# Kernel optimization log

Measured on AMD Instinct MI355X. Metric: run time of the kernel, lower is better.

Reference implementation:

```python
import jax, jax.numpy as jnp
import numpy as np

D_MODEL = 1024


def setup_inputs() -> dict:
    key = jax.random.key(0)
    ks = jax.random.split(key, 7)
    x = jax.random.normal(ks[0], (4, 2048, D_MODEL), dtype=jnp.float32)
    scale = 1.0 / np.sqrt(D_MODEL)
    Wq = jax.random.normal(ks[1], (D_MODEL, D_MODEL), dtype=jnp.float32) * scale
    bq = jnp.zeros((D_MODEL,), dtype=jnp.float32)
    Wk = jax.random.normal(ks[2], (D_MODEL, D_MODEL), dtype=jnp.float32) * scale
    bk = jnp.zeros((D_MODEL,), dtype=jnp.float32)
    Wv = jax.random.normal(ks[3], (D_MODEL, D_MODEL), dtype=jnp.float32) * scale
    bv = jnp.zeros((D_MODEL,), dtype=jnp.float32)
    return {"x": x, "Wq": Wq, "bq": bq, "Wk": Wk, "bk": bk, "Wv": Wv, "bv": bv}


def reference(x, Wq, bq, Wk, bk, Wv, bv):
    # Linear layers: y = x @ W^T + b (torch nn.Linear convention)
    q = jnp.einsum("bsd,ed->bse", x, Wq) + bq
    k = jnp.einsum("bsd,ed->bse", x, Wk) + bk
    v = jnp.einsum("bsd,ed->bse", x, Wv) + bv
    d_k = q.shape[-1]
    inv_sqrt_dk = 1.0 / jnp.sqrt(jnp.float32(d_k))
    # [B, S, S] score matrix, softmax over keys, then AV
    score = jnp.einsum("bqd,bkd->bqk", q, k) * inv_sqrt_dk
    attn = jax.nn.softmax(score, axis=-1)
    out = jnp.einsum("bqk,bkd->bqd", attn, v)
    return out
```

## Files before the change

### kernel.cpp

```cpp
#include <hip/hip_runtime.h>
#include <hip/hip_bf16.h>


typedef __hip_bfloat16 bf16;
typedef __attribute__((ext_vector_type(8))) short bf16x8;
typedef __attribute__((ext_vector_type(4))) float f32x4;
typedef __attribute__((ext_vector_type(4))) short short4v;

__device__ __forceinline__ void gload16(const bf16* g, bf16* l) {
  __builtin_amdgcn_global_load_lds(
      (const __attribute__((address_space(1))) void*)g,
      (__attribute__((address_space(3))) void*)l, 16, 0, 0);
}

__global__ __launch_bounds__(256)
void cast_f32_to_bf16(const float* __restrict__ in, bf16* __restrict__ out) {
  long i = ((long)blockIdx.x * blockDim.x + threadIdx.x) * 4;
  float4 f = *(const float4*)(in + i);
  bf16 tmp[4];
  tmp[0] = __float2bfloat16(f.x);
  tmp[1] = __float2bfloat16(f.y);
  tmp[2] = __float2bfloat16(f.z);
  tmp[3] = __float2bfloat16(f.w);
  *(short4v*)(out + i) = *(short4v*)tmp;
}

__global__ __launch_bounds__(256)
void cast3_f32_to_bf16(const float* __restrict__ w0, const float* __restrict__ w1,
                       const float* __restrict__ w2, bf16* __restrict__ out) {
  const float* src = (blockIdx.y == 0) ? w0 : (blockIdx.y == 1) ? w1 : w2;
  long i = ((long)blockIdx.x * blockDim.x + threadIdx.x) * 4;
  float4 f = *(const float4*)(src + i);
  bf16 tmp[4];
  tmp[0] = __float2bfloat16(f.x);
  tmp[1] = __float2bfloat16(f.y);
  tmp[2] = __float2bfloat16(f.z);
  tmp[3] = __float2bfloat16(f.w);
  *(short4v*)(out + (long)blockIdx.y * 1024 * 1024 + i) = *(short4v*)tmp;
}

template<int OMODE>
__global__ __launch_bounds__(256, 3)
void gemm_bt(const bf16* __restrict__ A, const bf16* __restrict__ Bt,
             const float* __restrict__ b0, const float* __restrict__ b1,
             const float* __restrict__ b2, void* __restrict__ Cout,
             int K, int lda, int ldb, int ldc, float scale,
             long sA, long sB, long sC)
{
  __shared__ __align__(16) bf16 As[128 * 64];
  __shared__ __align__(16) bf16 Bs[128 * 64];
  const int tid = threadIdx.x;
  const int z = blockIdx.z;
  const bf16* Ab = A + (long)z * sA;
  const bf16* Bb = Bt + (long)z * sB;
  const long bm = (long)blockIdx.x * 128;
  const long bn = (long)blockIdx.y * 128;
  const int wid = tid >> 6;
  const int lane = tid & 63;
  const int wr = (wid >> 1) * 64;
  const int wc = (wid & 1) * 64;
  const int l15 = lane & 15;
  const int kg = lane >> 4;

  f32x4 acc[4][4];
#pragma unroll
  for (int m = 0; m < 4; ++m)
#pragma unroll
    for (int n = 0; n < 4; ++n)
      acc[m][n] = (f32x4){0.f, 0.f, 0.f, 0.f};

  for (int k0 = 0; k0 < K; k0 += 64) {
#pragma unroll
    for (int i = 0; i < 4; ++i) {
      const int c = (i << 8) + tid;
      const int r = c >> 3;
      const int j = (c & 7) ^ (r & 7);
      const int ldsch = (i << 8) + (wid << 6);
      gload16(Ab + (long)(bm + r) * lda + k0 + (j << 3), As + ldsch * 8);
      gload16(Bb + (long)(bn + r) * ldb + k0 + (j << 3), Bs + ldsch * 8);
    }
    __syncthreads();
#pragma unroll
    for (int kk = 0; kk < 2; ++kk) {
      bf16x8 af[4], bfv[4];
#pragma unroll
      for (int m = 0; m < 4; ++m) {
        const int row_l = wr + (m << 4) + l15;
        const int js = ((kk << 2) + kg) ^ (row_l & 7);
        af[m] = *(const bf16x8*)&As[(row_l << 6) + (js << 3)];
      }
#pragma unroll
      for (int n = 0; n < 4; ++n) {
        const int row_l = wc + (n << 4) + l15;
        const int js = ((kk << 2) + kg) ^ (row_l & 7);
        bfv[n] = *(const bf16x8*)&Bs[(row_l << 6) + (js << 3)];
      }
#pragma unroll
      for (int m = 0; m < 4; ++m)
#pragma unroll
        for (int n = 0; n < 4; ++n)
          acc[m][n] = __builtin_amdgcn_mfma_f32_16x16x32_bf16(
              af[m], bfv[n], acc[m][n], 0, 0, 0);
    }
    __syncthreads();
  }

#pragma unroll
  for (int m = 0; m < 4; ++m) {
    const long row0 = bm + wr + (m << 4) + (kg << 2);
#pragma unroll
    for (int n = 0; n < 4; ++n) {
      const long col = bn + wc + (n << 4) + l15;
      if constexpr (OMODE == 0) {
        float* C = (float*)Cout + (long)z * sC;
#pragma unroll
        for (int rr = 0; rr < 4; ++rr)
          C[(row0 + rr) * ldc + col] = acc[m][n][rr] * scale;
      } else if constexpr (OMODE == 1) {
        bf16* C = (bf16*)Cout + (long)z * sC;
#pragma unroll
        for (int rr = 0; rr < 4; ++rr)
          C[(row0 + rr) * ldc + col] = __float2bfloat16(acc[m][n][rr] * scale);
      } else {
        const float* bias = (z == 0) ? b0 : (z == 1) ? b1 : b2;
        const float bias_v = bias[col];
        if (z < 2) {
          bf16* C = (bf16*)Cout + (long)z * 8192 * 1024;
#pragma unroll
          for (int rr = 0; rr < 4; ++rr)
            C[(row0 + rr) * 1024 + col] =
                __float2bfloat16(acc[m][n][rr] + bias_v);
        } else {
          bf16* C = (bf16*)Cout + 2L * 8192 * 1024;
          const long bb = row0 >> 11;
          const long s0 = row0 & 2047;
          bf16 tmp[4];
#pragma unroll
          for (int rr = 0; rr < 4; ++rr)
            tmp[rr] = __float2bfloat16(acc[m][n][rr] + bias_v);
          *(short4v*)&C[(bb * 1024 + col) * 2048 + s0] = *(short4v*)tmp;
        }
      }
    }
  }
}

__global__ __launch_bounds__(256)
void softmax_bf16(bf16* __restrict__ S) {
  bf16* row = S + (size_t)blockIdx.x * 2048;
  const int tid = threadIdx.x;
  __shared__ float redA[4], redB[4];
  bf16x8 in = *(const bf16x8*)(row + (tid << 3));
  float v[8];
  float mx = -1e30f;
#pragma unroll
  for (int i = 0; i < 8; ++i) {
    v[i] = __bfloat162float(((const bf16*)&in)[i]);
    mx = fmaxf(mx, v[i]);
  }
#pragma unroll
  for (int o = 32; o; o >>= 1) mx = fmaxf(mx, __shfl_xor(mx, o));
  if ((tid & 63) == 0) redA[tid >> 6] = mx;
  __syncthreads();
  mx = fmaxf(fmaxf(redA[0], redA[1]), fmaxf(redA[2], redA[3]));
  float sum = 0.f;
#pragma unroll
  for (int i = 0; i < 8; ++i) {
    v[i] = __expf(v[i] - mx);
    sum += v[i];
  }
#pragma unroll
  for (int o = 32; o; o >>= 1) sum += __shfl_xor(sum, o);
  if ((tid & 63) == 0) redB[tid >> 6] = sum;
  __syncthreads();
  sum = redB[0] + redB[1] + redB[2] + redB[3];
  const float inv = 1.f / sum;
  bf16 tmp[8];
#pragma unroll
  for (int i = 0; i < 8; ++i) tmp[i] = __float2bfloat16(v[i] * inv);
  *(bf16x8*)(row + (tid << 3)) = *(bf16x8*)tmp;
}

extern "C" void kernel_launch(void* const* d_in, const int* in_sizes, int n_in,
                              void* d_out, int out_size, void* d_ws, size_t ws_size,
                              hipStream_t stream) {
  const float* x  = (const float*)d_in[0];
  const float* Wq = (const float*)d_in[1];
  const float* bq = (const float*)d_in[2];
  const float* Wk = (const float*)d_in[3];
  const float* bk = (const float*)d_in[4];
  const float* Wv = (const float*)d_in[5];
  const float* bv = (const float*)d_in[6];
  float* out = (float*)d_out;

  const int B = 4, S = 2048, D = 1024;
  const int M = B * S;

  bf16* xb  = (bf16*)d_ws;
  bf16* wqb = xb + (size_t)M * D;
  bf16* qb  = wqb + 3 * (size_t)D * D;
  bf16* kb  = qb + (size_t)M * D;
  bf16* vtb = kb + (size_t)M * D;
  bf16* sc  = vtb + (size_t)M * D;

  size_t avail = ws_size - ((size_t)((char*)sc - (char*)d_ws));
  int nb = (int)(avail / ((size_t)S * S * 2));
  if (nb > B) nb = B;
  if (nb < 1) nb = 1;

  cast_f32_to_bf16<<<dim3(M * D / 1024), 256, 0, stream>>>(x, xb);
  cast3_f32_to_bf16<<<dim3(D * D / 1024, 3), 256, 0, stream>>>(Wq, Wk, Wv, wqb);

  gemm_bt<3><<<dim3(M / 128, D / 128, 3), 256, 0, stream>>>(
      xb, wqb, bq, bk, bv, qb, D, D, D, D, 1.f, 0, (long)D * D, 0);

  const float iscale = 1.0f / 32.0f;
  for (int g = 0; g < B; g += nb) {
    const int gn = (g + nb <= B) ? nb : (B - g);
    gemm_bt<1><<<dim3(S / 128, S / 128, gn), 256, 0, stream>>>(
        qb + (size_t)g * S * D, kb + (size_t)g * S * D, nullptr, nullptr, nullptr,
        sc, D, D, D, S, iscale, (long)S * D, (long)S * D, (long)S * S);
    softmax_bf16<<<dim3(gn * S), 256, 0, stream>>>(sc);
    gemm_bt<0><<<dim3(S / 128, D / 128, gn), 256, 0, stream>>>(
        sc, vtb + (size_t)g * D * S, nullptr, nullptr, nullptr,
        out + (size_t)g * S * D, S, S, S, D, 1.f,
        (long)S * S, (long)D * S, (long)S * D);
  }
}
```

Measured before the change: 169.7 us.

## Triple-buffer GEMM with 256x128 tiles and 512-thread blocks

Replaces the single-buffered 128x128 GEMM with a 256x128-tile kernel that uses 8 waves and a three-stage LDS ring. Global-to-LDS loads for tile t+2 are issued before computing tile t, with explicit vmcnt waits and barriers, so memory latency overlaps MFMA work. The QKV projection now runs as one flat grid over the concatenated 3*D output columns rather than a z-batched launch. The cost is 144KB of LDS per block, which limits occupancy to one block per CU. Each wave also now handles an 8x2 MFMA fragment layout with less B reuse.

```diff
diff --git a/kernel.cpp b/kernel.cpp
--- a/kernel.cpp
+++ b/kernel.cpp
@@ -12,6 +12,10 @@
       (const __attribute__((address_space(1))) void*)g,
       (__attribute__((address_space(3))) void*)l, 16, 0, 0);
 }
+
+#define WAITV(N) asm volatile("s_waitcnt vmcnt(" #N ")" ::: "memory")
+#define SCHED0   __builtin_amdgcn_sched_barrier(0)
+#define BAR      __builtin_amdgcn_s_barrier()
 
 __global__ __launch_bounds__(256)
 void cast_f32_to_bf16(const float* __restrict__ in, bf16* __restrict__ out) {
@@ -40,97 +44,127 @@
 }
 
 template<int OMODE>
-__global__ __launch_bounds__(256, 3)
-void gemm_bt(const bf16* __restrict__ A, const bf16* __restrict__ Bt,
-             const float* __restrict__ b0, const float* __restrict__ b1,
-             const float* __restrict__ b2, void* __restrict__ Cout,
-             int K, int lda, int ldb, int ldc, float scale,
-             long sA, long sB, long sC)
+__global__ __launch_bounds__(512)
+void gemm3s(const bf16* __restrict__ A, const bf16* __restrict__ Bt,
+            void* __restrict__ Cout, int K, int lda, int ldb, int ldc,
+            float scale, long sA, long sB, long sC,
+            const float* __restrict__ b0, const float* __restrict__ b1,
+            const float* __restrict__ b2)
 {
-  __shared__ __align__(16) bf16 As[128 * 64];
-  __shared__ __align__(16) bf16 Bs[128 * 64];
+  __shared__ __align__(16) bf16 As[3][256 * 64];
+  __shared__ __align__(16) bf16 Bs[3][128 * 64];
   const int tid = threadIdx.x;
+  const int wid = tid >> 6, lane = tid & 63;
+  const int l15 = lane & 15, kg = lane >> 4;
+  const int wr = (wid >> 2) * 128;
+  const int wc = (wid & 3) * 32;
   const int z = blockIdx.z;
   const bf16* Ab = A + (long)z * sA;
   const bf16* Bb = Bt + (long)z * sB;
-  const long bm = (long)blockIdx.x * 128;
+  const long bm = (long)blockIdx.x * 256;
   const long bn = (long)blockIdx.y * 128;
-  const int wid = tid >> 6;
-  const int lane = tid & 63;
-  const int wr = (wid >> 1) * 64;
-  const int wc = (wid & 1) * 64;
-  const int l15 = lane & 15;
-  const int kg = lane >> 4;
-
-  f32x4 acc[4][4];
-#pragma unroll
-  for (int m = 0; m < 4; ++m)
-#pragma unroll
-    for (int n = 0; n < 4; ++n)
+
+  const bf16* gA[4]; int dA[4];
+  const bf16* gB[2]; int dB[2];
+#pragma unroll
+  for (int i = 0; i < 4; ++i) {
+    const int c = (i << 9) + tid;
+    const int r = c >> 3;
+    const int j = (c & 7) ^ (r & 7);
+    gA[i] = Ab + (long)(bm + r) * lda + (j << 3);
+    dA[i] = ((i << 9) + (wid << 6)) << 3;
+  }
+#pragma unroll
+  for (int i = 0; i < 2; ++i) {
+    const int c = (i << 9) + tid;
+    const int r = c >> 3;
+    const int j = (c & 7) ^ (r & 7);
+    gB[i] = Bb + (long)(bn + r) * ldb + (j << 3);
+    dB[i] = ((i << 9) + (wid << 6)) << 3;
+  }
+
+#define STAGE(BUF, TT) do { const int _ko = (TT) << 6;          \
+    gload16(gA[0] + _ko, As[BUF] + dA[0]);                      \
+    gload16(gA[1] + _ko, As[BUF] + dA[1]);                      \
+    gload16(gA[2] + _ko, As[BUF] + dA[2]);                      \
+    gload16(gA[3] + _ko, As[BUF] + dA[3]);                      \
+    gload16(gB[0] + _ko, Bs[BUF] + dB[0]);                      \
+    gload16(gB[1] + _ko, Bs[BUF] + dB[1]); } while (0)
+
+  f32x4 acc[8][2];
+#pragma unroll
+  for (int m = 0; m < 8; ++m)
+#pragma unroll
+    for (int n = 0; n < 2; ++n)
       acc[m][n] = (f32x4){0.f, 0.f, 0.f, 0.f};
 
-  for (int k0 = 0; k0 < K; k0 += 64) {
-#pragma unroll
-    for (int i = 0; i < 4; ++i) {
-      const int c = (i << 8) + tid;
-      const int r = c >> 3;
-      const int j = (c & 7) ^ (r & 7);
-      const int ldsch = (i << 8) + (wid << 6);
-      gload16(Ab + (long)(bm + r) * lda + k0 + (j << 3), As + ldsch * 8);
-      gload16(Bb + (long)(bn + r) * ldb + k0 + (j << 3), Bs + ldsch * 8);
-    }
-    __syncthreads();
+  const int T = K >> 6;
+  STAGE(0, 0);
+  STAGE(1, 1);
+  int rb = 0;
+  for (int t = 0; t < T; ++t) {
+    int sb = rb + 2; if (sb >= 3) sb -= 3;
+    if (t + 2 < T) { STAGE(sb, t + 2); WAITV(12); }
+    else if (t + 1 < T) { WAITV(6); }
+    else { WAITV(0); }
+    SCHED0; BAR; SCHED0;
+    const bf16* Ac = As[rb];
+    const bf16* Bc = Bs[rb];
 #pragma unroll
     for (int kk = 0; kk < 2; ++kk) {
-      bf16x8 af[4], bfv[4];
-#pragma unroll
-      for (int m = 0; m < 4; ++m) {
+      bf16x8 af[8], bv[2];
+#pragma unroll
+      for (int m = 0; m < 8; ++m) {
         const int row_l = wr + (m << 4) + l15;
         const int js = ((kk << 2) + kg) ^ (row_l & 7);
-        af[m] = *(const bf16x8*)&As[(row_l << 6) + (js << 3)];
+        af[m] = *(const bf16x8*)&Ac[(row_l << 6) + (js << 3)];
       }
 #pragma unroll
-      for (int n = 0; n < 4; ++n) {
+      for (int n = 0; n < 2; ++n) {
         const int row_l = wc + (n << 4) + l15;
         const int js = ((kk << 2) + kg) ^ (row_l & 7);
-        bfv[n] = *(const bf16x8*)&Bs[(row_l << 6) + (js << 3)];
+        bv[n] = *(const bf16x8*)&Bc[(row_l << 6) + (js << 3)];
       }
 #pragma unroll
-      for (int m = 0; m < 4; ++m)
-#pragma unroll
-        for (int n = 0; n < 4; ++n)
+      for (int m = 0; m < 8; ++m)
+#pragma unroll
+        for (int n = 0; n < 2; ++n)
           acc[m][n] = __builtin_amdgcn_mfma_f32_16x16x32_bf16(
-              af[m], bfv[n], acc[m][n], 0, 0, 0);
+              af[m], bv[n], acc[m][n], 0, 0, 0);
     }
-    __syncthreads();
-  }
-
-#pragma unroll
-  for (int m = 0; m < 4; ++m) {
+    SCHED0; BAR;
+    rb = (rb + 1 == 3) ? 0 : rb + 1;
+  }
+#undef STAGE
+
+#pragma unroll
+  for (int m = 0; m < 8; ++m) {
     const long row0 = bm + wr + (m << 4) + (kg << 2);
 #pragma unroll
-    for (int n = 0; n < 4; ++n) {
+    for (int n = 0; n < 2; ++n) {
       const long col = bn + wc + (n << 4) + l15;
       if constexpr (OMODE == 0) {
         float* C = (float*)Cout + (long)z * sC;
 #pragma unroll
         for (int rr = 0; rr < 4; ++rr)
           C[(row0 + rr) * ldc + col] = acc[m][n][rr] * scale;
-      } else if constexpr (OMODE == 1) {
+      } else if constexpr (OMODE == 2) {
         bf16* C = (bf16*)Cout + (long)z * sC;
 #pragma unroll
         for (int rr = 0; rr < 4; ++rr)
           C[(row0 + rr) * ldc + col] = __float2bfloat16(acc[m][n][rr] * scale);
       } else {
-        const float* bias = (z == 0) ? b0 : (z == 1) ? b1 : b2;
-        const float bias_v = bias[col];
-        if (z < 2) {
-          bf16* C = (bf16*)Cout + (long)z * 8192 * 1024;
+        const int mat = (int)(col >> 10);
+        const long c1 = col & 1023;
+        if (mat < 2) {
+          const float bias_v = (mat ? b1 : b0)[c1];
+          bf16* C = (bf16*)Cout + (long)mat * 8192 * 1024;
 #pragma unroll
           for (int rr = 0; rr < 4; ++rr)
-            C[(row0 + rr) * 1024 + col] =
+            C[(row0 + rr) * 1024 + c1] =
                 __float2bfloat16(acc[m][n][rr] + bias_v);
         } else {
+          const float bias_v = b2[c1];
           bf16* C = (bf16*)Cout + 2L * 8192 * 1024;
           const long bb = row0 >> 11;
           const long s0 = row0 & 2047;
@@ -138,7 +172,7 @@
 #pragma unroll
           for (int rr = 0; rr < 4; ++rr)
             tmp[rr] = __float2bfloat16(acc[m][n][rr] + bias_v);
-          *(short4v*)&C[(bb * 1024 + col) * 2048 + s0] = *(short4v*)tmp;
+          *(short4v*)&C[(bb * 1024 + c1) * 2048 + s0] = *(short4v*)tmp;
         }
       }
     }
@@ -211,19 +245,21 @@
   cast_f32_to_bf16<<<dim3(M * D / 1024), 256, 0, stream>>>(x, xb);
   cast3_f32_to_bf16<<<dim3(D * D / 1024, 3), 256, 0, stream>>>(Wq, Wk, Wv, wqb);
 
-  gemm_bt<3><<<dim3(M / 128, D / 128, 3), 256, 0, stream>>>(
-      xb, wqb, bq, bk, bv, qb, D, D, D, D, 1.f, 0, (long)D * D, 0);
+  gemm3s<1><<<dim3(M / 256, 3 * D / 128, 1), 512, 0, stream>>>(
+      xb, wqb, qb, D, D, D, 0, 1.f, 0, 0, 0, bq, bk, bv);
 
   const float iscale = 1.0f / 32.0f;
   for (int g = 0; g < B; g += nb) {
     const int gn = (g + nb <= B) ? nb : (B - g);
-    gemm_bt<1><<<dim3(S / 128, S / 128, gn), 256, 0, stream>>>(
-        qb + (size_t)g * S * D, kb + (size_t)g * S * D, nullptr, nullptr, nullptr,
-        sc, D, D, D, S, iscale, (long)S * D, (long)S * D, (long)S * S);
+    gemm3s<2><<<dim3(S / 256, S / 128, gn), 512, 0, stream>>>(
+        qb + (size_t)g * S * D, kb + (size_t)g * S * D,
+        sc, D, D, D, S, iscale, (long)S * D, (long)S * D, (long)S * S,
+        nullptr, nullptr, nullptr);
     softmax_bf16<<<dim3(gn * S), 256, 0, stream>>>(sc);
-    gemm_bt<0><<<dim3(S / 128, D / 128, gn), 256, 0, stream>>>(
-        sc, vtb + (size_t)g * D * S, nullptr, nullptr, nullptr,
+    gemm3s<0><<<dim3(S / 256, D / 128, gn), 512, 0, stream>>>(
+        sc, vtb + (size_t)g * D * S,
         out + (size_t)g * S * D, S, S, S, D, 1.f,
-        (long)S * S, (long)D * S, (long)S * D);
-  }
-}
+        (long)S * S, (long)D * S, (long)S * D,
+        nullptr, nullptr, nullptr);
+  }
+}
```

New measurement: 210.8 us. 24.2% more time.
